# Optimization experiments

Measured on AMD Instinct MI355X. Metric: run time of the kernel, lower is better.

The kernel has to match this reference:

```python
import jax, jax.numpy as jnp
import numpy as np

N = 4096      # nodes
E = 131072    # edges (before self loops)
C = 512       # channels
H = 8         # heads
CO = C // H   # per-head out channels (64)
EPS = 1e-5
NEG_SLOPE = 0.2


def layer_norm(x, g, b):
    mu = jnp.mean(x, axis=-1, keepdims=True)
    var = jnp.mean((x - mu) ** 2, axis=-1, keepdims=True)
    return (x - mu) * jax.lax.rsqrt(var + EPS) * g + b


def gatv2(x, src, dst, wl, bl, wr, br, att, bias):
    # PyG GATv2Conv, concat=True, add_self_loops handled by caller.
    n = x.shape[0]
    xl = (x @ wl.T + bl).reshape(n, H, CO)   # target-side features
    xr = (x @ wr.T + br).reshape(n, H, CO)   # source-side features (messages)
    e = jax.nn.leaky_relu(xl[dst] + xr[src], NEG_SLOPE)   # [E+N, H, CO]
    alpha = jnp.einsum('ehc,hc->eh', e, att)              # [E+N, H]
    # segment softmax over destination neighborhoods
    amax = jax.ops.segment_max(alpha, dst, num_segments=n)
    ex = jnp.exp(alpha - amax[dst])
    denom = jax.ops.segment_sum(ex, dst, num_segments=n)
    a = ex / denom[dst]                                   # [E+N, H]
    msg = xr[src] * a[:, :, None]                         # [E+N, H, CO]
    out = jax.ops.segment_sum(msg, dst, num_segments=n)   # [N, H, CO]
    return out.reshape(n, H * CO) + bias


def mha(x, in_w, in_b, out_w, out_b):
    # nn.MultiheadAttention self-attention, batch=1, eval mode
    n = x.shape[0]
    qkv = x @ in_w.T + in_b                               # [N, 3C]
    q, k, v = jnp.split(qkv, 3, axis=-1)
    q = q.reshape(n, H, CO); k = k.reshape(n, H, CO); v = v.reshape(n, H, CO)
    scores = jnp.einsum('qhd,khd->hqk', q, k) / jnp.sqrt(jnp.float32(CO))
    p = jax.nn.softmax(scores, axis=-1)
    o = jnp.einsum('hqk,khd->qhd', p, v).reshape(n, C)
    return o @ out_w.T + out_b


def setup_inputs() -> dict:
    key = jax.random.key(0)
    ks = jax.random.split(key, 24)
    s = 0.02
    d = {}
    d['x'] = jax.random.normal(ks[0], (N, C), jnp.float32)
    d['edge_index'] = jax.random.randint(ks[1], (2, E), 0, N, dtype=jnp.int64)
    d['gat_wl'] = jax.random.normal(ks[2], (H * CO, C), jnp.float32) * s
    d['gat_bl'] = jnp.zeros((H * CO,), jnp.float32)
    d['gat_wr'] = jax.random.normal(ks[3], (H * CO, C), jnp.float32) * s
    d['gat_br'] = jnp.zeros((H * CO,), jnp.float32)
    d['gat_att'] = jax.random.normal(ks[4], (H, CO), jnp.float32) * s
    d['gat_b'] = jnp.zeros((H * CO,), jnp.float32)
    d['in_w'] = jax.random.normal(ks[5], (3 * C, C), jnp.float32) * s
    d['in_b'] = jnp.zeros((3 * C,), jnp.float32)
    d['out_w'] = jax.random.normal(ks[6], (C, C), jnp.float32) * s
    d['out_b'] = jnp.zeros((C,), jnp.float32)
    d['ln1_g'] = jnp.ones((C,), jnp.float32); d['ln1_b'] = jnp.zeros((C,), jnp.float32)
    d['ln2_g'] = jnp.ones((C,), jnp.float32); d['ln2_b'] = jnp.zeros((C,), jnp.float32)
    d['ln3_g'] = jnp.ones((C,), jnp.float32); d['ln3_b'] = jnp.zeros((C,), jnp.float32)
    d['w1'] = jax.random.normal(ks[7], (4 * C, C), jnp.float32) * s
    d['b1'] = jnp.zeros((4 * C,), jnp.float32)
    d['w2'] = jax.random.normal(ks[8], (C, 4 * C), jnp.float32) * s
    d['b2'] = jnp.zeros((C,), jnp.float32)
    return d


def reference(x, edge_index, gat_wl, gat_bl, gat_wr, gat_br, gat_att, gat_b,
              in_w, in_b, out_w, out_b, ln1_g, ln1_b, ln2_g, ln2_b,
              ln3_g, ln3_b, w1, b1, w2, b2):
    n = x.shape[0]
    loops = jnp.arange(n, dtype=edge_index.dtype)
    src = jnp.concatenate([edge_index[0], loops])
    dst = jnp.concatenate([edge_index[1], loops])
    h_local = gatv2(x, src, dst, gat_wl, gat_bl, gat_wr, gat_br, gat_att, gat_b)
    x = layer_norm(x + h_local, ln1_g, ln1_b)
    h_global = mha(x, in_w, in_b, out_w, out_b)
    x = layer_norm(x + h_global, ln2_g, ln2_b)
    h_ffn = (jax.nn.gelu(x @ w1.T + b1, approximate=False)) @ w2.T + b2
    x = layer_norm(x + h_ffn, ln3_g, ln3_b)
    return x
```

## Files before the change

kernel.cpp:

```cpp
#include <hip/hip_runtime.h>
#include <math.h>

#define NN 4096
#define CC 512
#define EE 131072
#define NEDGE (EE + NN)
#define HH 8
#define DCO 64
#define NC2 2097152L

typedef __attribute__((ext_vector_type(8))) short bfrag;
typedef __attribute__((ext_vector_type(4))) float f32x4;
typedef __attribute__((ext_vector_type(4))) int i32x4;

__device__ __forceinline__ float bf2f(unsigned short u) {
  union { float f; unsigned int i; } x; x.i = ((unsigned int)u) << 16; return x.f;
}
__device__ __forceinline__ unsigned short f2bf(float f) {
  union { float f; unsigned int i; } x; x.f = f;
  unsigned int r = x.i + 0x7FFFu + ((x.i >> 16) & 1u);
  return (unsigned short)(r >> 16);
}
__device__ __forceinline__ unsigned short f2bf_trunc(float f) {
  union { float f; unsigned int i; } x; x.f = f;
  return (unsigned short)(x.i >> 16);
}

__device__ __forceinline__ void gld16(const unsigned short* g, unsigned short* l) {
  __builtin_amdgcn_global_load_lds(
      (__attribute__((address_space(1))) unsigned int*)g,
      (__attribute__((address_space(3))) unsigned int*)l, 16, 0, 0);
}

#define QSC 0.18033688011112042f

#define CX  2097152L
#define CWL (CX + 262144L)
#define CWR (CWL + 262144L)
#define CIW (CWR + 786432L)
#define COW (CIW + 262144L)
#define CW1 (COW + 1048576L)
#define CW2 (CW1 + 1048576L)

__global__ void cvt_all(const float* __restrict__ x, const float* __restrict__ wl,
                        const float* __restrict__ wr, const float* __restrict__ iw,
                        const float* __restrict__ ow, const float* __restrict__ w1,
                        const float* __restrict__ w2, unsigned short* __restrict__ dst) {
  long i = ((long)blockIdx.x * 256 + threadIdx.x) * 4;
  if (i >= CW2) return;
  const float* s; long o;
  if (i < CX)       { s = x;  o = i; }
  else if (i < CWL) { s = wl; o = i - CX; }
  else if (i < CWR) { s = wr; o = i - CWL; }
  else if (i < CIW) { s = iw; o = i - CWR; }
  else if (i < COW) { s = ow; o = i - CIW; }
  else if (i < CW1) { s = w1; o = i - COW; }
  else              { s = w2; o = i - CW1; }
  f32x4 v = *(const f32x4*)(s + o);
  union { unsigned long long q; unsigned short u[4]; } t;
#pragma unroll
  for (int j = 0; j < 4; j++) t.u[j] = f2bf(v[j]);
  *(unsigned long long*)(dst + i) = t.q;
}

template<int OMODE, int TN, bool SPLIT>
__global__ __launch_bounds__(256) void gemm_t(
    const unsigned short* __restrict__ A, const unsigned short* __restrict__ B,
    const float* __restrict__ bias, void* __restrict__ C,
    int K, int lda, int ldb, int ldc)
{
  __shared__ unsigned short As[4096];
  __shared__ unsigned short Bs[TN * 32];
  constexpr int MI = (TN == 128) ? 4 : 2;
  const int tid = threadIdx.x;
  const int wave = tid >> 6, lane = tid & 63;
  const int ml = lane & 15, kq = lane >> 4;
  const int wm = (TN == 128) ? ((wave >> 1) << 6) : (wave << 5);
  const int wn = (TN == 128) ? ((wave & 1) << 6) : 0;
  const int bm = blockIdx.y << 7, bn = blockIdx.x * TN;
  const int srow = tid >> 2, scol = (tid & 3) << 3;
  if (SPLIT) { A += (long)blockIdx.z * K; B += (long)blockIdx.z * K; }
  const float* biasp = (!SPLIT || blockIdx.z == 0) ? bias : nullptr;
  const unsigned short* Ag = A + (long)(bm + srow) * lda + scol;
  const unsigned short* Bg = B + (long)(bn + srow) * ldb + scol;
  const long astep = (long)64 * lda, bstep = (long)64 * ldb;
  unsigned short* lA0 = As + tid * 8;
  unsigned short* lA1 = As + 2048 + tid * 8;
  unsigned short* lB0 = Bs + tid * 8;
  f32x4 acc[MI][4];
#pragma unroll
  for (int mi = 0; mi < MI; mi++)
#pragma unroll
    for (int ni = 0; ni < 4; ni++) acc[mi][ni] = (f32x4){0.f, 0.f, 0.f, 0.f};
  for (int k0 = 0; k0 < K; k0 += 32) {
    __syncthreads();
    gld16(Ag, lA0); gld16(Ag + astep, lA1);
    gld16(Bg, lB0);
    if (TN == 128) gld16(Bg + bstep, Bs + 2048 + tid * 8);
    Ag += 32; Bg += 32;
    __syncthreads();
    bfrag af[MI], bf[4];
#pragma unroll
    for (int mi = 0; mi < MI; mi++)
      af[mi] = *(const bfrag*)&As[(wm + (mi << 4) + ml) * 32 + (kq << 3)];
#pragma unroll
    for (int ni = 0; ni < 4; ni++)
      bf[ni] = *(const bfrag*)&Bs[(wn + (ni << 4) + ml) * 32 + (kq << 3)];
#pragma unroll
    for (int mi = 0; mi < MI; mi++)
#pragma unroll
      for (int ni = 0; ni < 4; ni++)
        acc[mi][ni] = __builtin_amdgcn_mfma_f32_16x16x32_bf16(af[mi], bf[ni], acc[mi][ni], 0, 0, 0);
  }
#pragma unroll
  for (int ni = 0; ni < 4; ni++) {
    int col = bn + wn + (ni << 4) + ml;
    float bb = biasp ? biasp[col] : 0.f;
#pragma unroll
    for (int mi = 0; mi < MI; mi++) {
      int row0 = bm + wm + (mi << 4) + (kq << 2);
#pragma unroll
      for (int r = 0; r < 4; r++) {
        float v = acc[mi][ni][r] + bb;
        int row = row0 + r;
        if (OMODE == 3) {
          unsigned short* q = (unsigned short*)C;
          if (col < 512) {
            int h = col >> 6, d = col & 63;
            q[(long)h * (NN * DCO) + (long)row * DCO + d] = f2bf(v * QSC);
          } else if (col < 1024) {
            int c2 = col - 512, h = c2 >> 6, d = c2 & 63;
            q[NC2 + (long)h * (NN * DCO) + (long)row * DCO + d] = f2bf(v);
          } else {
            int c2 = col - 1024, h = c2 >> 6, d = c2 & 63;
            q[2 * NC2 + (long)h * (DCO * NN) + (long)d * NN + row] = f2bf(v);
          }
        } else if (OMODE == 0) {
          long off = (SPLIT ? (long)blockIdx.z * NC2 : 0) + (long)row * ldc + col;
          ((float*)C)[off] = v;
        } else {
          if (OMODE == 2) v = 0.5f * v * (1.f + erff(v * 0.70710678118f));
          ((unsigned short*)C)[(long)row * ldc + col] = f2bf(v);
        }
      }
    }
  }
}

__global__ void count_k(const int* __restrict__ ei, int* __restrict__ cnt) {
  int e = blockIdx.x * 256 + threadIdx.x;
  if (e >= NEDGE) return;
  int d = (e < EE) ? ei[EE + e] : (e - EE);
  atomicAdd(&cnt[d], 1);
}

__global__ void scan_k(const int* __restrict__ cnt, int* __restrict__ rowptr) {
  __shared__ int s[1024];
  int t = threadIdx.x;
  int b = t * 4;
  int c0 = cnt[b], c1 = cnt[b + 1], c2 = cnt[b + 2], c3 = cnt[b + 3];
  int sum = c0 + c1 + c2 + c3;
  s[t] = sum;
  __syncthreads();
  for (int o = 1; o < 1024; o <<= 1) {
    int v = (t >= o) ? s[t - o] : 0;
    __syncthreads();
    s[t] += v;
    __syncthreads();
  }
  int ex = s[t] - sum;
  rowptr[b] = ex; rowptr[b + 1] = ex + c0;
  rowptr[b + 2] = ex + c0 + c1; rowptr[b + 3] = ex + c0 + c1 + c2;
  if (t == 1023) rowptr[4096] = ex + sum;
}

__global__ void scatter_k(const int* __restrict__ ei, const int* __restrict__ rowptr,
                          int* __restrict__ cur, int* __restrict__ order) {
  int e = blockIdx.x * 256 + threadIdx.x;
  if (e >= NEDGE) return;
  int d = (e < EE) ? ei[EE + e] : (e - EE);
  int p = atomicAdd(&cur[d], 1);
  order[rowptr[d] + p] = e;
}

__global__ __launch_bounds__(256) void gat_alpha(
    const unsigned short* __restrict__ xlr, const int* __restrict__ order,
    const int* __restrict__ ei, const float* __restrict__ att,
    float* __restrict__ alpha)
{
  int i = (blockIdx.x << 2) + (threadIdx.x >> 6);
  int e = order[i];
  int lane = threadIdx.x & 63;
  int src, dst;
  if (e < EE) { src = ei[e]; dst = ei[EE + e]; } else { src = dst = e - EE; }
  int c = lane << 3;
  union { i32x4 v; unsigned short u[8]; } L, R;
  L.v = *(const i32x4*)(xlr + (long)dst * 1024 + c);
  R.v = *(const i32x4*)(xlr + (long)src * 1024 + 512 + c);
  f32x4 t0 = *(const f32x4*)(att + c);
  f32x4 t1 = *(const f32x4*)(att + c + 4);
  float p = 0.f;
#pragma unroll
  for (int j = 0; j < 8; j++) {
    float x = bf2f(L.u[j]) + bf2f(R.u[j]);
    x = (x > 0.f) ? x : 0.2f * x;
    float tv = (j < 4) ? t0[j] : t1[j - 4];
    p += tv * x;
  }
  p += __shfl_xor(p, 1); p += __shfl_xor(p, 2); p += __shfl_xor(p, 4);
  if ((lane & 7) == 0) alpha[(long)i * 8 + (lane >> 3)] = p;
}

__global__ __launch_bounds__(256) void gat_aggr(
    const unsigned short* __restrict__ xlr, float* __restrict__ alpha,
    const int* __restrict__ order, const int* __restrict__ rowptr,
    const int* __restrict__ ei, const float* __restrict__ gbias,
    float* __restrict__ out)
{
  __shared__ float red[256];
  __shared__ float smax[8], sinv[8];
  __shared__ float part[4][512];
  int n = blockIdx.x, t = threadIdx.x;
  int beg = rowptr[n], deg = rowptr[n + 1] - beg;
  int h8 = t & 7, grp = t >> 3;
  float m = -1e30f;
  for (int i = grp; i < deg; i += 32)
    m = fmaxf(m, alpha[(long)(beg + i) * 8 + h8]);
  red[t] = m; __syncthreads();
  for (int off = 128; off >= 8; off >>= 1) {
    if (t < off) red[t] = fmaxf(red[t], red[t + off]);
    __syncthreads();
  }
  if (t < 8) smax[t] = red[t];
  __syncthreads();
  float mh = smax[h8];
  float s = 0.f;
  for (int i = grp; i < deg; i += 32) {
    long idx = (long)(beg + i) * 8 + h8;
    float ex = __expf(alpha[idx] - mh);
    alpha[idx] = ex;
    s += ex;
  }
  red[t] = s; __syncthreads();
  for (int off = 128; off >= 8; off >>= 1) {
    if (t < off) red[t] += red[t + off];
    __syncthreads();
  }
  if (t < 8) sinv[t] = 1.f / red[t];
  __syncthreads();
  int wave = t >> 6, lane = t & 63;
  int ch = lane << 3;
  int hh = lane >> 3;
  float acc[8];
#pragma unroll
  for (int j = 0; j < 8; j++) acc[j] = 0.f;
  for (int i = wave; i < deg; i += 4) {
    int e = order[beg + i];
    int sn = (e < EE) ? ei[e] : (e - EE);
    float wgt = alpha[(long)(beg + i) * 8 + hh];
    union { i32x4 v; unsigned short u[8]; } X;
    X.v = *(const i32x4*)(xlr + (long)sn * 1024 + 512 + ch);
#pragma unroll
    for (int j = 0; j < 8; j++) acc[j] += wgt * bf2f(X.u[j]);
  }
  *(f32x4*)&part[wave][ch]     = (f32x4){acc[0], acc[1], acc[2], acc[3]};
  *(f32x4*)&part[wave][ch + 4] = (f32x4){acc[4], acc[5], acc[6], acc[7]};
  __syncthreads();
#pragma unroll
  for (int c = t; c < 512; c += 256) {
    float v = part[0][c] + part[1][c] + part[2][c] + part[3][c];
    out[(long)n * CC + c] = v * sinv[c >> 6] + gbias[c];
  }
}

template<bool SUM2>
__global__ __launch_bounds__(256) void resid_ln(
    const float* __restrict__ a, const float* __restrict__ b,
    const float* __restrict__ g, const float* __restrict__ be,
    float* __restrict__ of, unsigned short* __restrict__ ob)
{
  __shared__ float sh[8];
  int row = blockIdx.x, t = threadIdx.x;
  long base = (long)row * CC;
  float b0 = b[base + t], b1 = b[base + t + 256];
  if (SUM2) { b0 += b[NC2 + base + t]; b1 += b[NC2 + base + t + 256]; }
  float v0 = a[base + t] + b0;
  float v1 = a[base + t + 256] + b1;
  float s = v0 + v1, ss = v0 * v0 + v1 * v1;
  for (int o = 32; o > 0; o >>= 1) { s += __shfl_down(s, o); ss += __shfl_down(ss, o); }
  int wave = t >> 6, lane = t & 63;
  if (lane == 0) { sh[wave] = s; sh[4 + wave] = ss; }
  __syncthreads();
  float S = sh[0] + sh[1] + sh[2] + sh[3];
  float SS = sh[4] + sh[5] + sh[6] + sh[7];
  float mean = S * (1.f / 512.f);
  float var = SS * (1.f / 512.f) - mean * mean;
  float rs = rsqrtf(var + 1e-5f);
  float y0 = (v0 - mean) * rs * g[t] + be[t];
  float y1 = (v1 - mean) * rs * g[t + 256] + be[t + 256];
  if (of) { of[base + t] = y0; of[base + t + 256] = y1; }
  if (ob) { ob[base + t] = f2bf(y0); ob[base + t + 256] = f2bf(y1); }
}

__global__ __launch_bounds__(256) void flash_attn(
    const unsigned short* __restrict__ qkvP, float* __restrict__ Op,
    float* __restrict__ Lp)
{
  __shared__ unsigned short QP[128 * 72];
  __shared__ unsigned short Ks[64 * 72];
  __shared__ unsigned short Vs[64 * 72];
  const int tid = threadIdx.x;
  const int wave = tid >> 6, lane = tid & 63;
  const int ml = lane & 15, kq = lane >> 4;
  const int h = blockIdx.x & 7, qt = blockIdx.x >> 3;
  const int sp = blockIdx.y;
  const int n0 = qt << 7;
  const unsigned short* Qh = qkvP + (long)h * (NN * DCO);
  const unsigned short* Kh = qkvP + NC2 + (long)h * (NN * DCO);
  const unsigned short* Vh = qkvP + 2 * NC2 + (long)h * (DCO * NN);
  {
    int r = tid >> 1, c = (tid & 1) << 5;
    const unsigned short* src = Qh + (long)(n0 + r) * DCO + c;
    unsigned short* d = &QP[r * 72 + c];
    *(i32x4*)d        = *(const i32x4*)src;
    *(i32x4*)(d + 8)  = *(const i32x4*)(src + 8);
    *(i32x4*)(d + 16) = *(const i32x4*)(src + 16);
    *(i32x4*)(d + 24) = *(const i32x4*)(src + 24);
  }
  __syncthreads();
  bfrag aq[2][2];
#pragma unroll
  for (int s = 0; s < 2; s++)
#pragma unroll
    for (int kh = 0; kh < 2; kh++)
      aq[s][kh] = *(const bfrag*)&QP[(wave * 32 + s * 16 + ml) * 72 + kh * 32 + (kq << 3)];
  bfrag ones;
#pragma unroll
  for (int j = 0; j < 8; j++) ones[j] = (short)0x3F80;
  f32x4 Oa[2][4];
  f32x4 Lc[2];
#pragma unroll
  for (int s = 0; s < 2; s++) {
    Lc[s] = (f32x4){0.f, 0.f, 0.f, 0.f};
#pragma unroll
    for (int dg = 0; dg < 4; dg++) Oa[s][dg] = (f32x4){0.f, 0.f, 0.f, 0.f};
  }
  const int r_ = tid >> 2, c_ = (tid & 3) << 4;
  const int j0 = sp << 4;
  i32x4 ka, kb, va, vb;
  {
    int k0 = j0 << 6;
    ka = *(const i32x4*)(Kh + (long)(k0 + r_) * DCO + c_);
    kb = *(const i32x4*)(Kh + (long)(k0 + r_) * DCO + c_ + 8);
    va = *(const i32x4*)(Vh + (long)r_ * NN + k0 + c_);
    vb = *(const i32x4*)(Vh + (long)r_ * NN + k0 + c_ + 8);
  }
  for (int jj = 0; jj < 16; jj++) {
    if (jj) __syncthreads();
    *(i32x4*)&Ks[r_ * 72 + c_] = ka; *(i32x4*)&Ks[r_ * 72 + c_ + 8] = kb;
    *(i32x4*)&Vs[r_ * 72 + c_] = va; *(i32x4*)&Vs[r_ * 72 + c_ + 8] = vb;
    __syncthreads();
    if (jj < 15) {
      int k0 = (j0 + jj + 1) << 6;
      ka = *(const i32x4*)(Kh + (long)(k0 + r_) * DCO + c_);
      kb = *(const i32x4*)(Kh + (long)(k0 + r_) * DCO + c_ + 8);
      va = *(const i32x4*)(Vh + (long)r_ * NN + k0 + c_);
      vb = *(const i32x4*)(Vh + (long)r_ * NN + k0 + c_ + 8);
    }
    f32x4 sc[2][4];
#pragma unroll
    for (int s = 0; s < 2; s++)
#pragma unroll
      for (int c = 0; c < 4; c++) sc[s][c] = (f32x4){0.f, 0.f, 0.f, 0.f};
#pragma unroll
    for (int c = 0; c < 4; c++) {
      bfrag bk0 = *(const bfrag*)&Ks[(c * 16 + ml) * 72 + (kq << 3)];
      bfrag bk1 = *(const bfrag*)&Ks[(c * 16 + ml) * 72 + 32 + (kq << 3)];
#pragma unroll
      for (int s = 0; s < 2; s++) {
        sc[s][c] = __builtin_amdgcn_mfma_f32_16x16x32_bf16(aq[s][0], bk0, sc[s][c], 0, 0, 0);
        sc[s][c] = __builtin_amdgcn_mfma_f32_16x16x32_bf16(aq[s][1], bk1, sc[s][c], 0, 0, 0);
      }
    }
#pragma unroll
    for (int s = 0; s < 2; s++)
#pragma unroll
      for (int c = 0; c < 4; c++)
#pragma unroll
        for (int r = 0; r < 4; r++) {
          float p = exp2f(sc[s][c][r]);
          QP[(wave * 32 + s * 16 + (kq << 2) + r) * 72 + c * 16 + ml] = f2bf_trunc(p);
        }
    bfrag ap[2][2];
#pragma unroll
    for (int s = 0; s < 2; s++)
#pragma unroll
      for (int kh = 0; kh < 2; kh++)
        ap[s][kh] = *(const bfrag*)&QP[(wave * 32 + s * 16 + ml) * 72 + kh * 32 + (kq << 3)];
#pragma unroll
    for (int s = 0; s < 2; s++) {
      Lc[s] = __builtin_amdgcn_mfma_f32_16x16x32_bf16(ap[s][0], ones, Lc[s], 0, 0, 0);
      Lc[s] = __builtin_amdgcn_mfma_f32_16x16x32_bf16(ap[s][1], ones, Lc[s], 0, 0, 0);
    }
#pragma unroll
    for (int dg = 0; dg < 4; dg++) {
      bfrag bv0 = *(const bfrag*)&Vs[(dg * 16 + ml) * 72 + (kq << 3)];
      bfrag bv1 = *(const bfrag*)&Vs[(dg * 16 + ml) * 72 + 32 + (kq << 3)];
#pragma unroll
      for (int s = 0; s < 2; s++) {
        Oa[s][dg] = __builtin_amdgcn_mfma_f32_16x16x32_bf16(ap[s][0], bv0, Oa[s][dg], 0, 0, 0);
        Oa[s][dg] = __builtin_amdgcn_mfma_f32_16x16x32_bf16(ap[s][1], bv1, Oa[s][dg], 0, 0, 0);
      }
    }
  }
  long obase = (long)sp * NC2;
#pragma unroll
  for (int s = 0; s < 2; s++)
#pragma unroll
    for (int dg = 0; dg < 4; dg++)
#pragma unroll
      for (int r = 0; r < 4; r++) {
        int row = wave * 32 + s * 16 + (kq << 2) + r;
        Op[obase + (long)(n0 + row) * CC + (h << 6) + (dg << 4) + ml] = Oa[s][dg][r];
      }
  if (ml == 0) {
#pragma unroll
    for (int s = 0; s < 2; s++)
#pragma unroll
      for (int r = 0; r < 4; r++) {
        int row = wave * 32 + s * 16 + (kq << 2) + r;
        Lp[(long)sp * (NN * HH) + (long)(n0 + row) * HH + h] = Lc[s][r];
      }
  }
}

__global__ void flash_combine(const float* __restrict__ Op, const float* __restrict__ Lp,
                              unsigned short* __restrict__ Ao) {
  int idx = blockIdx.x * 256 + threadIdx.x;
  int n = idx >> 9, c = idx & 511, h = c >> 6;
  float l = 0.f, o = 0.f;
#pragma unroll
  for (int s = 0; s < 4; s++) {
    l += Lp[(long)s * (NN * HH) + (long)n * HH + h];
    o += Op[(long)s * NC2 + idx];
  }
  Ao[idx] = f2bf(o / l);
}

extern "C" void kernel_launch(void* const* d_in, const int* in_sizes, int n_in,
                              void* d_out, int out_size, void* d_ws, size_t ws_size,
                              hipStream_t stream) {
  typedef unsigned short u16;
  const float* x      = (const float*)d_in[0];
  const int*   ei     = (const int*)d_in[1];
  const float* wl     = (const float*)d_in[2];
  const float* bl     = (const float*)d_in[3];
  const float* wr     = (const float*)d_in[4];
  const float* br     = (const float*)d_in[5];
  const float* att    = (const float*)d_in[6];
  const float* gat_b  = (const float*)d_in[7];
  const float* in_w   = (const float*)d_in[8];
  const float* in_b   = (const float*)d_in[9];
  const float* out_w  = (const float*)d_in[10];
  const float* out_b  = (const float*)d_in[11];
  const float* ln1g   = (const float*)d_in[12];
  const float* ln1b   = (const float*)d_in[13];
  const float* ln2g   = (const float*)d_in[14];
  const float* ln2b   = (const float*)d_in[15];
  const float* ln3g   = (const float*)d_in[16];
  const float* ln3b   = (const float*)d_in[17];
  const float* w1     = (const float*)d_in[18];
  const float* b1     = (const float*)d_in[19];
  const float* w2     = (const float*)d_in[20];
  const float* b2     = (const float*)d_in[21];

  const size_t MB = 1u << 20;
  char* w = (char*)d_ws;
  float* h_f32   = (float*)(w + 0);
  float* x2_f32  = (float*)(w + 8 * MB);
  int*   cnt     = (int*)(w + 16 * MB);
  int*   rowptr  = (int*)(w + 16 * MB + 32 * 1024);
  int*   order   = (int*)(w + 16 * MB + 64 * 1024);
  u16*   cvt     = (u16*)(w + 17 * MB);
  u16*   xbf     = cvt;
  u16*   wlrbf   = cvt + CX;
  u16*   inwbf   = cvt + CWR;
  u16*   outwbf  = cvt + CIW;
  u16*   w1bf    = cvt + COW;
  u16*   w2bf    = cvt + CW1;
  u16*   xlr_bf  = (u16*)(w + 29 * MB);
  float* alpha   = (float*)(w + 37 * MB);
  float* gat_out = (float*)(w + 42 * MB);
  float* Opart   = (float*)(w + 29 * MB);
  float* proj    = (float*)(w + 29 * MB);
  u16*   ffn1    = (u16*)(w + 45 * MB);
  u16*   qkvP    = (u16*)(w + 93 * MB);
  float* biasc   = (float*)(w + 105 * MB);
  float* Lpart   = (float*)(w + 105 * MB);
  u16*   Ao      = (u16*)(w + 106 * MB);
  u16*   actb    = (u16*)(w + 110 * MB);

  cvt_all<<<5632, 256, 0, stream>>>(x, wl, wr, in_w, out_w, w1, w2, cvt);
  hipMemsetAsync(cnt, 0, NN * sizeof(int), stream);
  count_k<<<(NEDGE + 255) / 256, 256, 0, stream>>>(ei, cnt);
  scan_k<<<1, 1024, 0, stream>>>(cnt, rowptr);
  hipMemsetAsync(cnt, 0, NN * sizeof(int), stream);
  scatter_k<<<(NEDGE + 255) / 256, 256, 0, stream>>>(ei, rowptr, cnt, order);

  hipMemcpyAsync(biasc, bl, 512 * sizeof(float), hipMemcpyDeviceToDevice, stream);
  hipMemcpyAsync(biasc + 512, br, 512 * sizeof(float), hipMemcpyDeviceToDevice, stream);
  gemm_t<1, 64, false><<<dim3(16, 32), 256, 0, stream>>>(xbf, wlrbf, biasc, xlr_bf, 512, 512, 512, 1024);
  gat_alpha<<<NEDGE / 4, 256, 0, stream>>>(xlr_bf, order, ei, att, alpha);
  gat_aggr<<<NN, 256, 0, stream>>>(xlr_bf, alpha, order, rowptr, ei, gat_b, gat_out);
  resid_ln<false><<<NN, 256, 0, stream>>>(x, gat_out, ln1g, ln1b, h_f32, actb);

  gemm_t<3, 64, false><<<dim3(24, 32), 256, 0, stream>>>(actb, inwbf, in_b, qkvP, 512, 512, 512, 0);
  flash_attn<<<dim3(256, 4), 256, 0, stream>>>(qkvP, Opart, Lpart);
  flash_combine<<<(NN * CC) / 256, 256, 0, stream>>>(Opart, Lpart, Ao);
  gemm_t<0, 64, true><<<dim3(8, 32, 2), 256, 0, stream>>>(Ao, outwbf, out_b, proj, 256, 512, 512, 512);
  resid_ln<true><<<NN, 256, 0, stream>>>(h_f32, proj, ln2g, ln2b, x2_f32, actb);

  gemm_t<2, 128, false><<<dim3(16, 32), 256, 0, stream>>>(actb, w1bf, b1, ffn1, 512, 512, 512, 2048);
  gemm_t<0, 64, true><<<dim3(8, 32, 2), 256, 0, stream>>>(ffn1, w2bf, b2, proj, 1024, 2048, 2048, 512);
  resid_ln<true><<<NN, 256, 0, stream>>>(x2_f32, proj, ln3g, ln3b, (float*)d_out, nullptr);
}
```

Baseline: 385.1 us.

## Load K/V fragments directly from global memory, drop shared staging and block syncs

The flash attention kernel no longer stages Q, K and V tiles through shared memory with block-wide barriers and register prefetch. Each wave now reads its MFMA operand fragments straight from global memory (relying on L1/L2 reuse across the four waves), and keeps only a small per-wave shared buffer for the probability tile. This removes the __syncthreads and LDS traffic and adds a launch-bounds occupancy hint, at the cost of redundant global/cache loads and no explicit software prefetch.

```diff
diff --git a/kernel.cpp b/kernel.cpp
--- a/kernel.cpp
+++ b/kernel.cpp
@@ -302,13 +302,11 @@
   if (ob) { ob[base + t] = f2bf(y0); ob[base + t + 256] = f2bf(y1); }
 }
 
-__global__ __launch_bounds__(256) void flash_attn(
+__global__ __launch_bounds__(256, 4) void flash_attn(
     const unsigned short* __restrict__ qkvP, float* __restrict__ Op,
     float* __restrict__ Lp)
 {
-  __shared__ unsigned short QP[128 * 72];
-  __shared__ unsigned short Ks[64 * 72];
-  __shared__ unsigned short Vs[64 * 72];
+  __shared__ unsigned short Ps[4][32 * 72];
   const int tid = threadIdx.x;
   const int wave = tid >> 6, lane = tid & 63;
   const int ml = lane & 15, kq = lane >> 4;
@@ -318,22 +316,13 @@
   const unsigned short* Qh = qkvP + (long)h * (NN * DCO);
   const unsigned short* Kh = qkvP + NC2 + (long)h * (NN * DCO);
   const unsigned short* Vh = qkvP + 2 * NC2 + (long)h * (DCO * NN);
-  {
-    int r = tid >> 1, c = (tid & 1) << 5;
-    const unsigned short* src = Qh + (long)(n0 + r) * DCO + c;
-    unsigned short* d = &QP[r * 72 + c];
-    *(i32x4*)d        = *(const i32x4*)src;
-    *(i32x4*)(d + 8)  = *(const i32x4*)(src + 8);
-    *(i32x4*)(d + 16) = *(const i32x4*)(src + 16);
-    *(i32x4*)(d + 24) = *(const i32x4*)(src + 24);
-  }
-  __syncthreads();
+  unsigned short* Pw = &Ps[wave][0];
   bfrag aq[2][2];
 #pragma unroll
   for (int s = 0; s < 2; s++)
 #pragma unroll
     for (int kh = 0; kh < 2; kh++)
-      aq[s][kh] = *(const bfrag*)&QP[(wave * 32 + s * 16 + ml) * 72 + kh * 32 + (kq << 3)];
+      aq[s][kh] = *(const bfrag*)(Qh + (long)(n0 + wave * 32 + s * 16 + ml) * DCO + kh * 32 + (kq << 3));
   bfrag ones;
 #pragma unroll
   for (int j = 0; j < 8; j++) ones[j] = (short)0x3F80;
@@ -345,58 +334,31 @@
 #pragma unroll
     for (int dg = 0; dg < 4; dg++) Oa[s][dg] = (f32x4){0.f, 0.f, 0.f, 0.f};
   }
-  const int r_ = tid >> 2, c_ = (tid & 3) << 4;
-  const int j0 = sp << 4;
-  i32x4 ka, kb, va, vb;
-  {
-    int k0 = j0 << 6;
-    ka = *(const i32x4*)(Kh + (long)(k0 + r_) * DCO + c_);
-    kb = *(const i32x4*)(Kh + (long)(k0 + r_) * DCO + c_ + 8);
-    va = *(const i32x4*)(Vh + (long)r_ * NN + k0 + c_);
-    vb = *(const i32x4*)(Vh + (long)r_ * NN + k0 + c_ + 8);
-  }
   for (int jj = 0; jj < 16; jj++) {
-    if (jj) __syncthreads();
-    *(i32x4*)&Ks[r_ * 72 + c_] = ka; *(i32x4*)&Ks[r_ * 72 + c_ + 8] = kb;
-    *(i32x4*)&Vs[r_ * 72 + c_] = va; *(i32x4*)&Vs[r_ * 72 + c_ + 8] = vb;
-    __syncthreads();
-    if (jj < 15) {
-      int k0 = (j0 + jj + 1) << 6;
-      ka = *(const i32x4*)(Kh + (long)(k0 + r_) * DCO + c_);
-      kb = *(const i32x4*)(Kh + (long)(k0 + r_) * DCO + c_ + 8);
-      va = *(const i32x4*)(Vh + (long)r_ * NN + k0 + c_);
-      vb = *(const i32x4*)(Vh + (long)r_ * NN + k0 + c_ + 8);
-    }
-    f32x4 sc[2][4];
-#pragma unroll
-    for (int s = 0; s < 2; s++)
-#pragma unroll
-      for (int c = 0; c < 4; c++) sc[s][c] = (f32x4){0.f, 0.f, 0.f, 0.f};
+    const int k0 = ((sp << 4) + jj) << 6;
 #pragma unroll
     for (int c = 0; c < 4; c++) {
-      bfrag bk0 = *(const bfrag*)&Ks[(c * 16 + ml) * 72 + (kq << 3)];
-      bfrag bk1 = *(const bfrag*)&Ks[(c * 16 + ml) * 72 + 32 + (kq << 3)];
-#pragma unroll
-      for (int s = 0; s < 2; s++) {
-        sc[s][c] = __builtin_amdgcn_mfma_f32_16x16x32_bf16(aq[s][0], bk0, sc[s][c], 0, 0, 0);
-        sc[s][c] = __builtin_amdgcn_mfma_f32_16x16x32_bf16(aq[s][1], bk1, sc[s][c], 0, 0, 0);
+      const unsigned short* kp = Kh + (long)(k0 + c * 16 + ml) * DCO + (kq << 3);
+      bfrag bk0 = *(const bfrag*)kp;
+      bfrag bk1 = *(const bfrag*)(kp + 32);
+      f32x4 s0 = (f32x4){0.f, 0.f, 0.f, 0.f};
+      f32x4 s1 = (f32x4){0.f, 0.f, 0.f, 0.f};
+      s0 = __builtin_amdgcn_mfma_f32_16x16x32_bf16(aq[0][0], bk0, s0, 0, 0, 0);
+      s0 = __builtin_amdgcn_mfma_f32_16x16x32_bf16(aq[0][1], bk1, s0, 0, 0, 0);
+      s1 = __builtin_amdgcn_mfma_f32_16x16x32_bf16(aq[1][0], bk0, s1, 0, 0, 0);
+      s1 = __builtin_amdgcn_mfma_f32_16x16x32_bf16(aq[1][1], bk1, s1, 0, 0, 0);
+#pragma unroll
+      for (int r = 0; r < 4; r++) {
+        Pw[((kq << 2) + r) * 72 + c * 16 + ml]        = f2bf_trunc(exp2f(s0[r]));
+        Pw[(16 + (kq << 2) + r) * 72 + c * 16 + ml]   = f2bf_trunc(exp2f(s1[r]));
       }
     }
+    bfrag ap[2][2];
 #pragma unroll
     for (int s = 0; s < 2; s++)
 #pragma unroll
-      for (int c = 0; c < 4; c++)
-#pragma unroll
-        for (int r = 0; r < 4; r++) {
-          float p = exp2f(sc[s][c][r]);
-          QP[(wave * 32 + s * 16 + (kq << 2) + r) * 72 + c * 16 + ml] = f2bf_trunc(p);
-        }
-    bfrag ap[2][2];
-#pragma unroll
-    for (int s = 0; s < 2; s++)
-#pragma unroll
       for (int kh = 0; kh < 2; kh++)
-        ap[s][kh] = *(const bfrag*)&QP[(wave * 32 + s * 16 + ml) * 72 + kh * 32 + (kq << 3)];
+        ap[s][kh] = *(const bfrag*)&Pw[(s * 16 + ml) * 72 + kh * 32 + (kq << 3)];
 #pragma unroll
     for (int s = 0; s < 2; s++) {
       Lc[s] = __builtin_amdgcn_mfma_f32_16x16x32_bf16(ap[s][0], ones, Lc[s], 0, 0, 0);
@@ -404,8 +366,9 @@
     }
 #pragma unroll
     for (int dg = 0; dg < 4; dg++) {
-      bfrag bv0 = *(const bfrag*)&Vs[(dg * 16 + ml) * 72 + (kq << 3)];
-      bfrag bv1 = *(const bfrag*)&Vs[(dg * 16 + ml) * 72 + 32 + (kq << 3)];
+      const unsigned short* vp = Vh + (long)(dg * 16 + ml) * NN + k0 + (kq << 3);
+      bfrag bv0 = *(const bfrag*)vp;
+      bfrag bv1 = *(const bfrag*)(vp + 32);
 #pragma unroll
       for (int s = 0; s < 2; s++) {
         Oa[s][dg] = __builtin_amdgcn_mfma_f32_16x16x32_bf16(ap[s][0], bv0, Oa[s][dg], 0, 0, 0);
```

Result: slower. 441.4 us (+14.6%).
